# Kernel optimization log

Measured on AMD Instinct MI355X. Metric: run time of the kernel, lower is better.

The kernel has to match this reference:

```python
import jax, jax.numpy as jnp
import numpy as np

N_TOKENS = 16384
MODEL_DIM = 2048
NUM_EXPERTS = 64
K = 2


def setup_inputs() -> dict:
    key = jax.random.key(0)
    k1, k2 = jax.random.split(key)
    inputs = jax.random.normal(k1, (N_TOKENS, MODEL_DIM), dtype=jnp.float32)
    # gate weight, torch Linear(model_dim, num_experts, bias=False) -> [E, D]
    wg_weight = jax.random.normal(k2, (NUM_EXPERTS, MODEL_DIM), dtype=jnp.float32) * 0.02
    return {"inputs": inputs, "wg_weight": wg_weight}


def reference(inputs, wg_weight):
    E = wg_weight.shape[0]
    # gate computed in fp32 (module casts input and keeps wg in float32)
    logits = jnp.einsum("nd,ed->ne", inputs.astype(jnp.float32), wg_weight)
    probs = jax.nn.softmax(logits, axis=-1)                      # [N, E]
    topk_probs, topk_indices = jax.lax.top_k(probs, K)           # [N, K]
    flat_idx = topk_indices.reshape(-1)                          # [N*K]
    # stable sort of expert ids over all (token, slot) pairs
    sort_ordering = jnp.argsort(flat_idx)                        # [N*K]
    # reverse permutation: reversed[sort_ordering[i]] = i
    ar = jnp.arange(flat_idx.shape[0], dtype=sort_ordering.dtype)
    reversed_ordering = jnp.zeros_like(sort_ordering).at[sort_ordering].set(ar)
    # map slot index back to token index
    token_order = sort_ordering // K
    # per-expert counts (== unique_consecutive counts scattered into [E])
    input_splits = jnp.bincount(flat_idx, length=E).astype(jnp.int64)
    # combine weights: renormalize top-k probs via softmax when k > 1
    if K > 1:
        combine_weights = jax.nn.softmax(topk_probs, axis=-1)
    else:
        combine_weights = topk_probs
    combine_weights = combine_weights.reshape(-1).astype(inputs.dtype)
    return token_order, reversed_ordering, combine_weights, input_splits, probs
```

## Files before the change

### kernel.cpp

```cpp
#include <hip/hip_runtime.h>
#include <math.h>

#define N_TOKENS    16384
#define MODEL_DIM   2048
#define NUM_EXPERTS 64
#define NK          (N_TOKENS * 2)

#define OFF_TOKEN_ORDER 0
#define OFF_REVERSED    (NK)
#define OFF_COMBINE     (2 * NK)
#define OFF_SPLITS      (3 * NK)
#define OFF_PROBS       (3 * NK + NUM_EXPERTS)

#define NSEG 256
#define NFRAG 16384

typedef _Float16 half8 __attribute__((ext_vector_type(8)));
typedef float    f32x4 __attribute__((ext_vector_type(4)));

__device__ __forceinline__ void glds16(const void* g, void* l) {
    __builtin_amdgcn_global_load_lds(
        (const __attribute__((address_space(1))) void*)g,
        (__attribute__((address_space(3))) void*)l, 16, 0, 0);
}

__global__ __launch_bounds__(256) void preconvert(
    const float* __restrict__ w, half8* __restrict__ WH, half8* __restrict__ WL,
    int* __restrict__ segHist)
{
    const int fr = blockIdx.x * 256 + threadIdx.x;
    const int lane = fr & 63;
    const int tile = (fr >> 6) & 3;
    const int kstep = fr >> 8;
    const int e = tile * 16 + (lane & 15);
    const int kb = kstep * 32 + (lane >> 4) * 8;
    const float* src = w + (size_t)e * MODEL_DIM + kb;
    const float4 w0 = *(const float4*)(src);
    const float4 w1 = *(const float4*)(src + 4);
    const float av[8] = {w0.x, w0.y, w0.z, w0.w, w1.x, w1.y, w1.z, w1.w};
    half8 hh, hl;
#pragma unroll
    for (int j = 0; j < 8; j++) {
        const float v = av[j] * 64.0f;
        const _Float16 h = (_Float16)v;
        hh[j] = h;
        hl[j] = (_Float16)((v - (float)h) * 4096.0f);
    }
    WH[fr] = hh;
    WL[fr] = hl;
    segHist[fr] = 0;
}

__global__ __launch_bounds__(256, 2) void gate_fused(
    const float* __restrict__ x, const half8* __restrict__ WH,
    const half8* __restrict__ WL, float* __restrict__ out,
    int* __restrict__ flat_idx, int* __restrict__ segHist)
{
    __shared__ alignas(16) unsigned char astage[4][3][2048];
    __shared__ double red[128 * 17];

    const int tid  = threadIdx.x;
    const int wv   = tid >> 6;
    const int lane = tid & 63;
    const int kh   = wv & 1;
    const int tg   = wv >> 1;
    const int t0   = blockIdx.x * 32;
    const int col  = lane & 15;
    const int kg   = lane >> 4;

    const int r3 = lane >> 3;
    const int pp = (lane & 7) ^ r3;
    const float* pA0 = x + (size_t)(t0 + tg * 16 + r3) * MODEL_DIM + kh * 1024 + pp * 4;
    const float* pA1 = x + (size_t)(t0 + tg * 16 + 8 + r3) * MODEL_DIM + kh * 1024 + pp * 4;
    unsigned char* mys = &astage[wv][0][0];

    const int rr  = col & 7;
    const int rb  = (col >> 3) * 1024 + rr * 128;
    const int ro0 = rb + (((2 * kg)     ^ rr) << 4);
    const int ro1 = rb + (((2 * kg + 1) ^ rr) << 4);

    const half8* pbh = WH + ((size_t)kh * 32 * 4) * 64 + lane;
    const half8* pbl = WL + ((size_t)kh * 32 * 4) * 64 + lane;

    f32x4 accH[4], accC[4];
    double accD[4][4];
#pragma unroll
    for (int t = 0; t < 4; t++) {
        accH[t] = (f32x4){0.f, 0.f, 0.f, 0.f};
        accC[t] = (f32x4){0.f, 0.f, 0.f, 0.f};
#pragma unroll
        for (int r = 0; r < 4; r++) accD[t][r] = 0.0;
    }

    half8 bhA[4], blA[4], bhB[4], blB[4];

    glds16(pA0, mys);
    glds16(pA1, mys + 1024);
    glds16(pA0 + 32, mys + 2048);
    glds16(pA1 + 32, mys + 2048 + 1024);
#pragma unroll
    for (int t = 0; t < 4; t++) {
        bhA[t] = pbh[t * 64];
        blA[t] = pbl[t * 64];
    }

    int j = 0, curb = 0, dstb = 2;

#define BODY(BHC, BLC, BHN, BLN) do {                                        \
    const int jn2 = (j < 30) ? (j + 2) : 31;                                 \
    glds16(pA0 + jn2 * 32, mys + dstb * 2048);                               \
    glds16(pA1 + jn2 * 32, mys + dstb * 2048 + 1024);                        \
    const half8* pbh_n = pbh + ((j < 31) ? 256 : 0);                         \
    const half8* pbl_n = pbl + ((j < 31) ? 256 : 0);                         \
    _Pragma("unroll")                                                        \
    for (int t_ = 0; t_ < 4; t_++) {                                         \
        BHN[t_] = pbh_n[t_ * 64];                                            \
        BLN[t_] = pbl_n[t_ * 64];                                            \
    }                                                                        \
    pbh = pbh_n; pbl = pbl_n;                                                \
    asm volatile("s_waitcnt vmcnt(10)" ::: "memory");                        \
    __builtin_amdgcn_sched_barrier(0);                                       \
    const float4 a0 = *(const float4*)(mys + curb * 2048 + ro0);             \
    const float4 a1 = *(const float4*)(mys + curb * 2048 + ro1);             \
    const float av_[8] = {a0.x, a0.y, a0.z, a0.w, a1.x, a1.y, a1.z, a1.w};   \
    half8 ah, al;                                                            \
    _Pragma("unroll")                                                        \
    for (int q_ = 0; q_ < 8; q_++) {                                         \
        const float v_ = av_[q_];                                            \
        const _Float16 h_ = (_Float16)v_;                                    \
        ah[q_] = h_;                                                         \
        al[q_] = (_Float16)((v_ - (float)h_) * 4096.0f);                     \
    }                                                                        \
    _Pragma("unroll")                                                        \
    for (int t_ = 0; t_ < 4; t_++) {                                         \
        accH[t_] = __builtin_amdgcn_mfma_f32_16x16x32_f16(ah, BHC[t_], accH[t_], 0, 0, 0); \
        accC[t_] = __builtin_amdgcn_mfma_f32_16x16x32_f16(ah, BLC[t_], accC[t_], 0, 0, 0); \
        accC[t_] = __builtin_amdgcn_mfma_f32_16x16x32_f16(al, BHC[t_], accC[t_], 0, 0, 0); \
    }                                                                        \
    if ((j & 7) == 7) {                                                      \
        _Pragma("unroll")                                                    \
        for (int t_ = 0; t_ < 4; t_++)                                       \
        _Pragma("unroll")                                                    \
        for (int r_ = 0; r_ < 4; r_++) {                                     \
            accD[t_][r_] += (double)accH[t_][r_] + (double)accC[t_][r_] * (1.0 / 4096.0); \
            accH[t_][r_] = 0.0f;                                             \
            accC[t_][r_] = 0.0f;                                             \
        }                                                                    \
    }                                                                        \
    curb = (curb == 2) ? 0 : curb + 1;                                       \
    dstb = (dstb == 2) ? 0 : dstb + 1;                                       \
    j++;                                                                     \
} while (0)

    for (int jj = 0; jj < 16; jj++) {
        BODY(bhA, blA, bhB, blB);
        BODY(bhB, blB, bhA, blA);
    }
#undef BODY

    asm volatile("s_waitcnt vmcnt(0)" ::: "memory");
    __syncthreads();

    if (kh == 1) {
#pragma unroll
        for (int t = 0; t < 4; t++)
#pragma unroll
            for (int r = 0; r < 4; r++)
                red[(tg * 64 + lane) * 17 + t * 4 + r] = accD[t][r];
    }
    __syncthreads();
    if (kh == 1) return;

#pragma unroll
    for (int t = 0; t < 4; t++)
#pragma unroll
        for (int r = 0; r < 4; r++)
            accD[t][r] += red[(tg * 64 + lane) * 17 + t * 4 + r];

    const int rowg = lane >> 4;
#pragma unroll
    for (int r = 0; r < 4; r++) {
        float lv[4];
#pragma unroll
        for (int t = 0; t < 4; t++) lv[t] = (float)(accD[t][r] * (1.0 / 64.0));

        float m = fmaxf(fmaxf(lv[0], lv[1]), fmaxf(lv[2], lv[3]));
#pragma unroll
        for (int d = 1; d < 16; d <<= 1) m = fmaxf(m, __shfl_xor(m, d));

        float l1 = -INFINITY, l2 = -INFINITY;
        int i1 = 0, i2 = 0;
#pragma unroll
        for (int t = 0; t < 4; t++) {
            const float l = lv[t];
            const int e = t * 16 + col;
            if (l > l1)      { l2 = l1; i2 = i1; l1 = l; i1 = e; }
            else if (l > l2) { l2 = l;  i2 = e; }
        }
#pragma unroll
        for (int d = 1; d < 16; d <<= 1) {
            const float ol1 = __shfl_xor(l1, d), ol2 = __shfl_xor(l2, d);
            const int   oi1 = __shfl_xor(i1, d), oi2 = __shfl_xor(i2, d);
            if (ol1 > l1 || (ol1 == l1 && oi1 < i1)) {
                if (l1 > ol2 || (l1 == ol2 && i1 < oi2)) { l2 = l1;  i2 = i1;  }
                else                                     { l2 = ol2; i2 = oi2; }
                l1 = ol1; i1 = oi1;
            } else if (ol1 > l2 || (ol1 == l2 && oi1 < i2)) {
                l2 = ol1; i2 = oi1;
            }
        }

        float ex[4];
        double sd = 0.0;
#pragma unroll
        for (int t = 0; t < 4; t++) { ex[t] = expf(lv[t] - m); sd += (double)ex[t]; }
#pragma unroll
        for (int d = 1; d < 16; d <<= 1) sd += __shfl_xor(sd, d);
        const float inv = (float)(1.0 / sd);

        const int tok = t0 + tg * 16 + rowg * 4 + r;
        float* pp2 = out + OFF_PROBS + (size_t)tok * NUM_EXPERTS + col;
#pragma unroll
        for (int t = 0; t < 4; t++) pp2[t * 16] = ex[t] * inv;

        if (col == 0) {
            const float p1 = expf(l1 - m) * inv;
            const float p2 = expf(l2 - m) * inv;
            const float e2 = expf(p2 - p1);
            const float rr2 = 1.0f / (1.0f + e2);
            out[OFF_COMBINE + 2 * tok]     = rr2;
            out[OFF_COMBINE + 2 * tok + 1] = e2 * rr2;
            flat_idx[2 * tok]     = i1;
            flat_idx[2 * tok + 1] = i2;
            atomicAdd(&segHist[(tok >> 6) * NUM_EXPERTS + i1], 1);
            atomicAdd(&segHist[(tok >> 6) * NUM_EXPERTS + i2], 1);
        }
    }
}

__global__ __launch_bounds__(256) void scan_scatter(
    const int* __restrict__ flat_idx, const int* __restrict__ segHist,
    float* __restrict__ out)
{
    __shared__ int h[NSEG * NUM_EXPERTS];
    __shared__ int gtot[4 * NUM_EXPERTS];
    __shared__ int base_[NUM_EXPERTS];
    __shared__ int cnt[2 * NUM_EXPERTS];

    const int tid = threadIdx.x;
    for (int i = tid; i < NSEG * NUM_EXPERTS / 4; i += 256)
        *(int4*)(h + i * 4) = *(const int4*)(segHist + i * 4);
    if (tid < 2 * NUM_EXPERTS) cnt[tid] = 0;
    __syncthreads();

    const int e = tid & 63;
    const int g = tid >> 6;
    int run = 0;
    for (int s = g * 64; s < g * 64 + 64; s++) {
        const int idx = s * NUM_EXPERTS + e;
        const int v = h[idx];
        h[idx] = run;
        run += v;
    }
    gtot[g * NUM_EXPERTS + e] = run;
    __syncthreads();

    if (tid < NUM_EXPERTS) {
        int b = 0;
#pragma unroll
        for (int gg = 0; gg < 4; gg++) {
            const int t = gtot[gg * NUM_EXPERTS + tid];
            gtot[gg * NUM_EXPERTS + tid] = b;
            b += t;
        }
        if (blockIdx.x == 0) out[OFF_SPLITS + tid] = (float)b;
        int xs = b;
#pragma unroll
        for (int off = 1; off < 64; off <<= 1) {
            const int v = __shfl_up(xs, off);
            if (tid >= off) xs += v;
        }
        base_[tid] = xs - b;
    }
    __syncthreads();

    const int i = blockIdx.x * 256 + tid;
    const int ee = flat_idx[i];
    const int lane = tid & 63;
    const int wv = tid >> 6;
    const int segslot = wv >> 1;
    const int seg = i >> 7;

    unsigned long long match = ~0ull;
#pragma unroll
    for (int b = 0; b < 6; b++) {
        const unsigned long long m = __ballot((ee >> b) & 1);
        match &= ((ee >> b) & 1) ? m : ~m;
    }
    const int rank = __popcll(match & ((1ull << lane) - 1ull));

    const int segoff = h[seg * NUM_EXPERTS + ee]
                     + gtot[(seg >> 6) * NUM_EXPERTS + ee] + base_[ee];

    int pos = 0;
    if ((wv & 1) == 0) {
        pos = segoff + rank;
        if (lane == __builtin_ctzll(match))
            cnt[segslot * NUM_EXPERTS + ee] = __popcll(match);
    }
    __syncthreads();
    if ((wv & 1) == 1)
        pos = segoff + cnt[segslot * NUM_EXPERTS + ee] + rank;

    out[OFF_TOKEN_ORDER + pos] = (float)(i >> 1);
    out[OFF_REVERSED + i]      = (float)pos;
}

extern "C" void kernel_launch(void* const* d_in, const int* in_sizes, int n_in,
                              void* d_out, int out_size, void* d_ws, size_t ws_size,
                              hipStream_t stream) {
    const float* x = (const float*)d_in[0];
    const float* w = (const float*)d_in[1];
    float* out = (float*)d_out;

    int* flat_idx = (int*)d_ws;
    int* segHist  = flat_idx + NK;
    half8* WH = (half8*)(segHist + NSEG * NUM_EXPERTS);
    half8* WL = WH + NFRAG;

    preconvert<<<64, 256, 0, stream>>>(w, WH, WL, segHist);
    gate_fused<<<512, 256, 0, stream>>>(x, WH, WL, out, flat_idx, segHist);
    scan_scatter<<<NK / 256, 256, 0, stream>>>(flat_idx, segHist, out);
}
```

Baseline: 226.2 us.

## Stage gate weights and activations in double-buffered LDS shared by 64-token blocks

The gate GEMM kernel now runs 512-thread blocks covering 64 tokens. Each wave loads one slice of the hi/lo fp16 weight fragments and the fp32 activation rows into registers, then writes them into a double-buffered LDS tile that every wave reads from. Previously each wave fetched its own weight fragments from global memory and staged activations through direct global-to-LDS loads. The aim is to cut redundant weight traffic by sharing it across four token groups and to overlap the next tile's loads with the MFMA work. In exchange it adds a block-wide barrier every k-step and more register staging, and it halves the grid to 256 blocks.

Measured after the change: 320.6 us. 41.8% more time.

```diff
diff --git a/kernel.cpp b/kernel.cpp
--- a/kernel.cpp
+++ b/kernel.cpp
@@ -15,14 +15,12 @@
 #define NSEG 256
 #define NFRAG 16384
 
+#define BUF_BYTES 32768
+
 typedef _Float16 half8 __attribute__((ext_vector_type(8)));
 typedef float    f32x4 __attribute__((ext_vector_type(4)));
 
-__device__ __forceinline__ void glds16(const void* g, void* l) {
-    __builtin_amdgcn_global_load_lds(
-        (const __attribute__((address_space(1))) void*)g,
-        (__attribute__((address_space(3))) void*)l, 16, 0, 0);
-}
+#define MEMFENCE asm volatile("" ::: "memory")
 
 __global__ __launch_bounds__(256) void preconvert(
     const float* __restrict__ w, half8* __restrict__ WH, half8* __restrict__ WL,
@@ -51,36 +49,51 @@
     segHist[fr] = 0;
 }
 
-__global__ __launch_bounds__(256, 2) void gate_fused(
+__global__ __launch_bounds__(512, 2) void gate_fused(
     const float* __restrict__ x, const half8* __restrict__ WH,
     const half8* __restrict__ WL, float* __restrict__ out,
     int* __restrict__ flat_idx, int* __restrict__ segHist)
 {
-    __shared__ alignas(16) unsigned char astage[4][3][2048];
-    __shared__ double red[128 * 17];
+    __shared__ alignas(16) unsigned char smem[2 * BUF_BYTES];
 
     const int tid  = threadIdx.x;
     const int wv   = tid >> 6;
     const int lane = tid & 63;
     const int kh   = wv & 1;
     const int tg   = wv >> 1;
-    const int t0   = blockIdx.x * 32;
+    const int t0   = blockIdx.x * 64;
     const int col  = lane & 15;
     const int kg   = lane >> 4;
 
-    const int r3 = lane >> 3;
-    const int pp = (lane & 7) ^ r3;
-    const float* pA0 = x + (size_t)(t0 + tg * 16 + r3) * MODEL_DIM + kh * 1024 + pp * 4;
-    const float* pA1 = x + (size_t)(t0 + tg * 16 + 8 + r3) * MODEL_DIM + kh * 1024 + pp * 4;
-    unsigned char* mys = &astage[wv][0][0];
-
-    const int rr  = col & 7;
-    const int rb  = (col >> 3) * 1024 + rr * 128;
-    const int ro0 = rb + (((2 * kg)     ^ rr) << 4);
-    const int ro1 = rb + (((2 * kg + 1) ^ rr) << 4);
-
-    const half8* pbh = WH + ((size_t)kh * 32 * 4) * 64 + lane;
-    const half8* pbl = WL + ((size_t)kh * 32 * 4) * 64 + lane;
+    const char* pSrc[4];
+    {
+        const int hl = wv & 1, tile = (wv >> 1) & 3;
+        pSrc[0] = (const char*)((hl ? WL : WH) + ((size_t)(0 * 128 + tile) * 64 + lane));
+        pSrc[1] = (const char*)((hl ? WL : WH) + ((size_t)(1 * 128 + tile) * 64 + lane));
+        const int row = t0 + wv * 8 + (lane >> 3);
+        pSrc[2] = (const char*)(x + (size_t)row * MODEL_DIM + (lane & 7) * 4);
+        pSrc[3] = (const char*)(x + (size_t)row * MODEL_DIM + 1024 + (lane & 7) * 4);
+    }
+    const int sStr[4] = {4096, 4096, 128, 128};
+    int dOff[4];
+    {
+        const int swz = (lane >> 3) * 128 + (((lane & 7) ^ (lane >> 3)) << 4);
+        dOff[0] = wv * 1024 + lane * 16;
+        dOff[1] = (wv + 8) * 1024 + lane * 16;
+        dOff[2] = (16 + wv) * 1024 + swz;
+        dOff[3] = (24 + wv) * 1024 + swz;
+    }
+
+    int bOff[8];
+#pragma unroll
+    for (int t = 0; t < 4; t++)
+#pragma unroll
+        for (int hl = 0; hl < 2; hl++)
+            bOff[t * 2 + hl] = (kh * 8 + t * 2 + hl) * 1024 + lane * 16;
+    const int chunkA = 16 + kh * 8 + tg * 2 + (col >> 3);
+    const int rowin  = col & 7;
+    const int aoff0  = chunkA * 1024 + rowin * 128 + (((2 * kg)     ^ rowin) << 4);
+    const int aoff1  = chunkA * 1024 + rowin * 128 + (((2 * kg + 1) ^ rowin) << 4);
 
     f32x4 accH[4], accC[4];
     double accD[4][4];
@@ -92,52 +105,46 @@
         for (int r = 0; r < 4; r++) accD[t][r] = 0.0;
     }
 
-    half8 bhA[4], blA[4], bhB[4], blB[4];
-
-    glds16(pA0, mys);
-    glds16(pA1, mys + 1024);
-    glds16(pA0 + 32, mys + 2048);
-    glds16(pA1 + 32, mys + 2048 + 1024);
-#pragma unroll
-    for (int t = 0; t < 4; t++) {
-        bhA[t] = pbh[t * 64];
-        blA[t] = pbl[t * 64];
-    }
-
-    int j = 0, curb = 0, dstb = 2;
-
-#define BODY(BHC, BLC, BHN, BLN) do {                                        \
-    const int jn2 = (j < 30) ? (j + 2) : 31;                                 \
-    glds16(pA0 + jn2 * 32, mys + dstb * 2048);                               \
-    glds16(pA1 + jn2 * 32, mys + dstb * 2048 + 1024);                        \
-    const half8* pbh_n = pbh + ((j < 31) ? 256 : 0);                         \
-    const half8* pbl_n = pbl + ((j < 31) ? 256 : 0);                         \
+    float4 RA[4], RB[4];
+
+#pragma unroll
+    for (int i = 0; i < 4; i++) RA[i] = *(const float4*)(pSrc[i]);
+#pragma unroll
+    for (int i = 0; i < 4; i++) RB[i] = *(const float4*)(pSrc[i] + sStr[i]);
+    asm volatile("s_waitcnt vmcnt(4)" ::: "memory");
+#pragma unroll
+    for (int i = 0; i < 4; i++) *(float4*)(smem + dOff[i]) = RA[i];
+
+#define ITER(RI, RW, CB, WB, T, DOFOLD) do {                                 \
+    const int jn_ = ((T) < 30) ? (T) + 2 : 31;                               \
     _Pragma("unroll")                                                        \
-    for (int t_ = 0; t_ < 4; t_++) {                                         \
-        BHN[t_] = pbh_n[t_ * 64];                                            \
-        BLN[t_] = pbl_n[t_ * 64];                                            \
-    }                                                                        \
-    pbh = pbh_n; pbl = pbl_n;                                                \
-    asm volatile("s_waitcnt vmcnt(10)" ::: "memory");                        \
-    __builtin_amdgcn_sched_barrier(0);                                       \
-    const float4 a0 = *(const float4*)(mys + curb * 2048 + ro0);             \
-    const float4 a1 = *(const float4*)(mys + curb * 2048 + ro1);             \
-    const float av_[8] = {a0.x, a0.y, a0.z, a0.w, a1.x, a1.y, a1.z, a1.w};   \
-    half8 ah, al;                                                            \
+    for (int i_ = 0; i_ < 4; i_++)                                           \
+        RI[i_] = *(const float4*)(pSrc[i_] + (size_t)jn_ * sStr[i_]);        \
+    asm volatile("s_waitcnt lgkmcnt(0)" ::: "memory");                       \
+    __builtin_amdgcn_s_barrier();                                            \
+    MEMFENCE;                                                                \
+    const unsigned char* buf_ = smem + (CB) * BUF_BYTES;                     \
+    const float4 a0_ = *(const float4*)(buf_ + aoff0);                       \
+    const float4 a1_ = *(const float4*)(buf_ + aoff1);                       \
+    const float av_[8] = {a0_.x, a0_.y, a0_.z, a0_.w,                        \
+                          a1_.x, a1_.y, a1_.z, a1_.w};                       \
+    half8 ah_, al_;                                                          \
     _Pragma("unroll")                                                        \
     for (int q_ = 0; q_ < 8; q_++) {                                         \
         const float v_ = av_[q_];                                            \
         const _Float16 h_ = (_Float16)v_;                                    \
-        ah[q_] = h_;                                                         \
-        al[q_] = (_Float16)((v_ - (float)h_) * 4096.0f);                     \
+        ah_[q_] = h_;                                                        \
+        al_[q_] = (_Float16)((v_ - (float)h_) * 4096.0f);                    \
     }                                                                        \
     _Pragma("unroll")                                                        \
     for (int t_ = 0; t_ < 4; t_++) {                                         \
-        accH[t_] = __builtin_amdgcn_mfma_f32_16x16x32_f16(ah, BHC[t_], accH[t_], 0, 0, 0); \
-        accC[t_] = __builtin_amdgcn_mfma_f32_16x16x32_f16(ah, BLC[t_], accC[t_], 0, 0, 0); \
-        accC[t_] = __builtin_amdgcn_mfma_f32_16x16x32_f16(al, BHC[t_], accC[t_], 0, 0, 0); \
+        const half8 bh_ = *(const half8*)(buf_ + bOff[t_ * 2]);              \
+        const half8 bl_ = *(const half8*)(buf_ + bOff[t_ * 2 + 1]);          \
+        accH[t_] = __builtin_amdgcn_mfma_f32_16x16x32_f16(ah_, bh_, accH[t_], 0, 0, 0); \
+        accC[t_] = __builtin_amdgcn_mfma_f32_16x16x32_f16(ah_, bl_, accC[t_], 0, 0, 0); \
+        accC[t_] = __builtin_amdgcn_mfma_f32_16x16x32_f16(al_, bh_, accC[t_], 0, 0, 0); \
     }                                                                        \
-    if ((j & 7) == 7) {                                                      \
+    if (DOFOLD) {                                                            \
         _Pragma("unroll")                                                    \
         for (int t_ = 0; t_ < 4; t_++)                                       \
         _Pragma("unroll")                                                    \
@@ -147,20 +154,23 @@
             accC[t_][r_] = 0.0f;                                             \
         }                                                                    \
     }                                                                        \
-    curb = (curb == 2) ? 0 : curb + 1;                                       \
-    dstb = (dstb == 2) ? 0 : dstb + 1;                                       \
-    j++;                                                                     \
+    asm volatile("s_waitcnt vmcnt(4)" ::: "memory");   \
+    unsigned char* wb_ = smem + (WB) * BUF_BYTES;                            \
+    _Pragma("unroll")                                                        \
+    for (int i_ = 0; i_ < 4; i_++) *(float4*)(wb_ + dOff[i_]) = RW[i_];      \
+    MEMFENCE;                                                                \
 } while (0)
 
-    for (int jj = 0; jj < 16; jj++) {
-        BODY(bhA, blA, bhB, blB);
-        BODY(bhB, blB, bhA, blA);
-    }
-#undef BODY
+    for (int tt = 0; tt < 16; tt++) {
+        ITER(RA, RB, 0, 1, 2 * tt,     false);
+        ITER(RB, RA, 1, 0, 2 * tt + 1, (tt & 3) == 3);
+    }
+#undef ITER
 
     asm volatile("s_waitcnt vmcnt(0)" ::: "memory");
     __syncthreads();
 
+    double* red = (double*)smem;
     if (kh == 1) {
 #pragma unroll
         for (int t = 0; t < 4; t++)
@@ -329,6 +339,6 @@
     half8* WL = WH + NFRAG;
 
     preconvert<<<64, 256, 0, stream>>>(w, WH, WL, segHist);
-    gate_fused<<<512, 256, 0, stream>>>(x, WH, WL, out, flat_idx, segHist);
+    gate_fused<<<256, 512, 0, stream>>>(x, WH, WL, out, flat_idx, segHist);
     scan_scatter<<<NK / 256, 256, 0, stream>>>(flat_idx, segHist, out);
 }
```
